# Optimization experiments

Measured on AMD Instinct MI355X. Metric: run time of the kernel, lower is better.

The kernel has to match this reference:

```python
import jax, jax.numpy as jnp
import numpy as np

NB_COMP, LAT_DIM, OUT_DIM, N = 16, 128, 512, 16384


def setup_inputs() -> dict:
    key = jax.random.key(0)
    ks = jax.random.split(key, 8)
    eps = jax.random.normal(ks[0], (N, LAT_DIM), dtype=jnp.float32)
    c = jax.random.randint(ks[1], (N,), 0, NB_COMP, dtype=jnp.int32)
    mu = jax.random.normal(ks[2], (NB_COMP, LAT_DIM), dtype=jnp.float32)
    sigma = jax.random.uniform(ks[3], (NB_COMP, LAT_DIM), dtype=jnp.float32)
    # Kaiming-ish init for the two expert linear layers
    W1 = jax.random.normal(ks[4], (NB_COMP, OUT_DIM, LAT_DIM), dtype=jnp.float32) / np.sqrt(LAT_DIM)
    b1 = jax.random.normal(ks[5], (NB_COMP, OUT_DIM), dtype=jnp.float32) * 0.01
    W2 = jax.random.normal(ks[6], (NB_COMP, OUT_DIM, OUT_DIM), dtype=jnp.float32) / np.sqrt(OUT_DIM)
    b2 = jax.random.normal(ks[7], (NB_COMP, OUT_DIM), dtype=jnp.float32) * 0.01
    return {"n": N, "eps": eps, "c": c, "mu": mu, "sigma": sigma,
            "W1": W1, "b1": b1, "W2": W2, "b2": b2}


def reference(n, eps, c, mu, sigma, W1, b1, W2, b2):
    # Per-sample latent from its component's mean-field variational dist:
    # lat[k] = eps[k] * sigma[c[k]] + mu[c[k]]
    lat = eps * sigma[c] + mu[c]                                  # (n, lat_dim)
    # Run every expert's 2-layer MLP densely, then select per-sample expert.
    hidden = jax.nn.relu(jnp.einsum("nd,chd->cnh", lat, W1) + b1[:, None, :])  # (C, n, H)
    out_all = jnp.einsum("cnh,cwh->cnw", hidden, W2) + b2[:, None, :]          # (C, n, W)
    return out_all[c, jnp.arange(n)]                              # (n, weights_dim)
```

## Files before the change

kernel.cpp:

```cpp
#include <hip/hip_runtime.h>

#define NB 16
#define LD 128
#define OD 512
#define NS 16384
#define NMB (NS/64 + NB)

typedef __attribute__((ext_vector_type(8))) short short8;
typedef __attribute__((ext_vector_type(4))) float f32x4;

#define WS_OFF     128
#define WS_POFF    256
#define WS_PERM    1024
#define WS_W1B     (128*1024)
#define WS_W2B     (WS_W1B + 2*1024*1024)
#define WS_HID     (WS_W2B + 8*1024*1024)

static __device__ __forceinline__ unsigned short f2bf(float f) {
  unsigned int u = __float_as_uint(f);
  u += 0x7FFFu + ((u >> 16) & 1u);
  return (unsigned short)(u >> 16);
}

#define SORT_T 1024
#define SORT_CH (NS / SORT_T)
__global__ __launch_bounds__(SORT_T) void k_sort(
    const int* __restrict__ c, int* __restrict__ off, int* __restrict__ poff,
    int* __restrict__ perm) {
  __shared__ int cnt[NB * SORT_T];
  __shared__ int totals[NB];
  __shared__ int ebase[NB];

  const int t = threadIdx.x;
  for (int e = 0; e < NB; ++e) cnt[e * SORT_T + t] = 0;
  __syncthreads();

  int myc[SORT_CH];
  for (int i = 0; i < SORT_CH; ++i) {
    int e = c[t * SORT_CH + i];
    myc[i] = e;
    cnt[e * SORT_T + t]++;
  }
  __syncthreads();

  const int w = t >> 6, l = t & 63;
  {
    int carry = 0;
    for (int chunk = 0; chunk < SORT_T / 64; ++chunk) {
      int idx = chunk * 64 + l;
      int v0 = cnt[w * SORT_T + idx];
      int v = v0;
      for (int d = 1; d < 64; d <<= 1) {
        int n = __shfl_up(v, d);
        if (l >= d) v += n;
      }
      cnt[w * SORT_T + idx] = carry + (v - v0);
      carry += __shfl(v, 63);
    }
    if (l == 0) totals[w] = carry;
  }
  __syncthreads();

  if (t == 0) {
    int o = 0, p = 0;
    for (int e = 0; e < NB; ++e) {
      off[e] = o; poff[e] = p; ebase[e] = o;
      o += totals[e];
      p += ((totals[e] + 63) >> 6) << 6;
    }
    off[NB] = o; poff[NB] = p;
  }
  __syncthreads();

  for (int i = 0; i < SORT_CH; ++i) {
    int e = myc[i];
    int pos = ebase[e] + cnt[e * SORT_T + t]++;
    perm[pos] = t * SORT_CH + i;
  }
}

__global__ void k_conv(const float* __restrict__ W1, const float* __restrict__ W2,
                       unsigned short* __restrict__ W1b, unsigned short* __restrict__ W2b) {
  const int n1 = NB * OD * LD / 4, n2 = NB * OD * OD / 4;
  for (int i = blockIdx.x * blockDim.x + threadIdx.x; i < n1 + n2;
       i += gridDim.x * blockDim.x) {
    float4 v; unsigned short* dst;
    if (i < n1) { v = ((const float4*)W1)[i]; dst = W1b + (size_t)i * 4; }
    else        { v = ((const float4*)W2)[i - n1]; dst = W2b + (size_t)(i - n1) * 4; }
    ushort4 o = make_ushort4(f2bf(v.x), f2bf(v.y), f2bf(v.z), f2bf(v.w));
    *(ushort4*)dst = o;
  }
}

__global__ __launch_bounds__(256) void k_gemm1(
    const float* __restrict__ eps, const float* __restrict__ mu,
    const float* __restrict__ sigma, const float* __restrict__ b1,
    const unsigned short* __restrict__ W1b,
    const int* __restrict__ off, const int* __restrict__ poff,
    const int* __restrict__ perm, unsigned short* __restrict__ hidden) {
  __shared__ alignas(16) unsigned short As[64 * 136];
  __shared__ alignas(16) unsigned short Bs[64 * 136];
  __shared__ alignas(16) float s_sig[LD];
  __shared__ alignas(16) float s_mu[LD];

  const int mt = blockIdx.y, ct = blockIdx.x;
  const int pr0 = mt * 64;
  if (pr0 >= poff[NB]) return;
  int e = 0;
  while (e < NB - 1 && poff[e + 1] <= pr0) e++;
  const int off_e = off[e];
  const int cnt   = off[e + 1] - off_e;
  const int l0    = pr0 - poff[e];

  const int t = threadIdx.x;
  if (t < LD) s_sig[t] = sigma[e * LD + t];
  else if (t < 2 * LD) s_mu[t - LD] = mu[e * LD + (t - LD)];
  __syncthreads();

  const int r = t >> 2, cseg = (t & 3) * 32;
  {
    int lrow = l0 + r;
    int k = (lrow < cnt) ? perm[off_e + lrow] : 0;
    const f32x4* eps4 = (const f32x4*)(eps + (size_t)k * LD + cseg);
    for (int j = 0; j < 8; ++j) {
      f32x4 v  = eps4[j];
      f32x4 sg = *(const f32x4*)(s_sig + cseg + j * 4);
      f32x4 m  = *(const f32x4*)(s_mu + cseg + j * 4);
      v = v * sg + m;
      ushort4 o = make_ushort4(f2bf(v[0]), f2bf(v[1]), f2bf(v[2]), f2bf(v[3]));
      *(ushort4*)(As + r * 136 + cseg + j * 4) = o;
    }
    const unsigned short* w1row =
        W1b + ((size_t)e * OD + ct * 64 + r) * LD + cseg;
    for (int j = 0; j < 4; ++j)
      *(uint4*)(Bs + r * 136 + cseg + j * 8) = *(const uint4*)(w1row + j * 8);
  }
  __syncthreads();

  const int lane = t & 63, w = t >> 6;
  const int wr = w >> 1, wc = w & 1;
  const int fr = lane & 15, fg = lane >> 4;
  f32x4 acc[2][2] = {};
  for (int ks = 0; ks < 4; ++ks) {
    short8 a[2], b[2];
    for (int fm = 0; fm < 2; ++fm)
      a[fm] = *(const short8*)(As + (wr * 32 + fm * 16 + fr) * 136 + ks * 32 + fg * 8);
    for (int fn = 0; fn < 2; ++fn)
      b[fn] = *(const short8*)(Bs + (wc * 32 + fn * 16 + fr) * 136 + ks * 32 + fg * 8);
    for (int fm = 0; fm < 2; ++fm)
      for (int fn = 0; fn < 2; ++fn)
        acc[fm][fn] = __builtin_amdgcn_mfma_f32_16x16x32_bf16(a[fm], b[fn], acc[fm][fn], 0, 0, 0);
  }

  const int colb = ct * 64 + wc * 32;
  float bv[2];
  bv[0] = b1[e * OD + colb + fr];
  bv[1] = b1[e * OD + colb + 16 + fr];
  for (int fm = 0; fm < 2; ++fm) {
    const int row0 = pr0 + wr * 32 + fm * 16 + fg * 4;
    for (int j = 0; j < 4; ++j)
      for (int fn = 0; fn < 2; ++fn) {
        float vv = acc[fm][fn][j] + bv[fn];
        vv = fmaxf(vv, 0.f);
        hidden[(size_t)(row0 + j) * OD + colb + fn * 16 + fr] = f2bf(vv);
      }
  }
}

__global__ __launch_bounds__(256) void k_gemm2(
    const float* __restrict__ b2, const unsigned short* __restrict__ W2b,
    const unsigned short* __restrict__ hidden,
    const int* __restrict__ off, const int* __restrict__ poff,
    const int* __restrict__ perm, float* __restrict__ out) {
  __shared__ alignas(16) unsigned short As[64 * 136];
  __shared__ alignas(16) unsigned short Bs[64 * 136];

  const int mt = blockIdx.y, ct = blockIdx.x;
  const int pr0 = mt * 64;
  if (pr0 >= poff[NB]) return;
  int e = 0;
  while (e < NB - 1 && poff[e + 1] <= pr0) e++;
  const int off_e = off[e];
  const int cnt   = off[e + 1] - off_e;
  const int l0    = pr0 - poff[e];

  const int t = threadIdx.x, r = t >> 2, cseg = (t & 3) * 32;
  const int lane = t & 63, w = t >> 6;
  const int wr = w >> 1, wc = w & 1;
  const int fr = lane & 15, fg = lane >> 4;

  f32x4 acc[2][2] = {};
  for (int kt = 0; kt < 4; ++kt) {
    const unsigned short* ap = hidden + (size_t)(pr0 + r) * OD + kt * 128 + cseg;
    const unsigned short* bp =
        W2b + ((size_t)e * OD + ct * 64 + r) * OD + kt * 128 + cseg;
    for (int j = 0; j < 4; ++j) {
      uint4 va = *(const uint4*)(ap + j * 8);
      uint4 vb = *(const uint4*)(bp + j * 8);
      *(uint4*)(As + r * 136 + cseg + j * 8) = va;
      *(uint4*)(Bs + r * 136 + cseg + j * 8) = vb;
    }
    __syncthreads();
    for (int ks = 0; ks < 4; ++ks) {
      short8 a[2], b[2];
      for (int fm = 0; fm < 2; ++fm)
        a[fm] = *(const short8*)(As + (wr * 32 + fm * 16 + fr) * 136 + ks * 32 + fg * 8);
      for (int fn = 0; fn < 2; ++fn)
        b[fn] = *(const short8*)(Bs + (wc * 32 + fn * 16 + fr) * 136 + ks * 32 + fg * 8);
      for (int fm = 0; fm < 2; ++fm)
        for (int fn = 0; fn < 2; ++fn)
          acc[fm][fn] = __builtin_amdgcn_mfma_f32_16x16x32_bf16(a[fm], b[fn], acc[fm][fn], 0, 0, 0);
    }
    __syncthreads();
  }

  const int colb = ct * 64 + wc * 32;
  float bv[2];
  bv[0] = b2[e * OD + colb + fr];
  bv[1] = b2[e * OD + colb + 16 + fr];
  for (int fm = 0; fm < 2; ++fm) {
    const int rl0 = wr * 32 + fm * 16 + fg * 4;
    for (int j = 0; j < 4; ++j) {
      const int lr = l0 + rl0 + j;
      if (lr < cnt) {
        const int k = perm[off_e + lr];
        for (int fn = 0; fn < 2; ++fn)
          out[(size_t)k * OD + colb + fn * 16 + fr] = acc[fm][fn][j] + bv[fn];
      }
    }
  }
}

extern "C" void kernel_launch(void* const* d_in, const int* in_sizes, int n_in,
                              void* d_out, int out_size, void* d_ws, size_t ws_size,
                              hipStream_t stream) {
  const float* eps   = (const float*)d_in[1];
  const int*   c     = (const int*)d_in[2];
  const float* mu    = (const float*)d_in[3];
  const float* sigma = (const float*)d_in[4];
  const float* W1    = (const float*)d_in[5];
  const float* b1    = (const float*)d_in[6];
  const float* W2    = (const float*)d_in[7];
  const float* b2    = (const float*)d_in[8];
  float* out = (float*)d_out;
  char*  ws  = (char*)d_ws;

  int* off     = (int*)(ws + WS_OFF);
  int* poff    = (int*)(ws + WS_POFF);
  int* perm    = (int*)(ws + WS_PERM);
  unsigned short* W1b = (unsigned short*)(ws + WS_W1B);
  unsigned short* W2b = (unsigned short*)(ws + WS_W2B);
  unsigned short* hid = (unsigned short*)(ws + WS_HID);

  k_sort<<<1, SORT_T, 0, stream>>>(c, off, poff, perm);
  k_conv<<<2048, 256, 0, stream>>>(W1, W2, W1b, W2b);
  k_gemm1<<<dim3(8, NMB), 256, 0, stream>>>(eps, mu, sigma, b1, W1b, off, poff, perm, hid);
  k_gemm2<<<dim3(8, NMB), 256, 0, stream>>>(b2, W2b, hid, off, poff, perm, out);
}
```

Before: 78.93 us.

## Use 128x128 tiles with direct global-to-LDS loads and a separate latent kernel

Grows each GEMM block tile from 64x64 to 128x128, with a 4x4 MFMA fragment grid per wave, and pads expert groups to 128 rows. Shared-memory tiles are now filled with global_load_lds instead of going through registers. The latent computation and gather move into a new k_lat kernel that writes permuted bf16 latents, so gemm1 becomes a plain tiled GEMM. The goal is more data reuse per block and less register traffic, at the cost of more padding rows, an extra launch and an unpadded, possibly bank-conflicting LDS layout.

Measured after the change: 71.69 us. -9.2%, faster.

```diff
diff --git a/kernel.cpp b/kernel.cpp
--- a/kernel.cpp
+++ b/kernel.cpp
@@ -4,7 +4,8 @@
 #define LD 128
 #define OD 512
 #define NS 16384
-#define NMB (NS/64 + NB)
+#define NPMAX (NS + NB*128)
+#define NMT (NPMAX/128)
 
 typedef __attribute__((ext_vector_type(8))) short short8;
 typedef __attribute__((ext_vector_type(4))) float f32x4;
@@ -15,6 +16,11 @@
 #define WS_W1B     (128*1024)
 #define WS_W2B     (WS_W1B + 2*1024*1024)
 #define WS_HID     (WS_W2B + 8*1024*1024)
+#define WS_LAT     (WS_HID + 20*1024*1024)
+
+#define GLDS16(g, l) __builtin_amdgcn_global_load_lds( \
+    (const __attribute__((address_space(1))) unsigned int*)(g), \
+    (__attribute__((address_space(3))) unsigned int*)(l), 16, 0, 0)
 
 static __device__ __forceinline__ unsigned short f2bf(float f) {
   unsigned int u = __float_as_uint(f);
@@ -66,7 +72,7 @@
     for (int e = 0; e < NB; ++e) {
       off[e] = o; poff[e] = p; ebase[e] = o;
       o += totals[e];
-      p += ((totals[e] + 63) >> 6) << 6;
+      p += ((totals[e] + 127) >> 7) << 7;
     }
     off[NB] = o; poff[NB] = p;
   }
@@ -92,19 +98,106 @@
   }
 }
 
+__global__ __launch_bounds__(256) void k_lat(
+    const float* __restrict__ eps, const float* __restrict__ mu,
+    const float* __restrict__ sigma,
+    const int* __restrict__ off, const int* __restrict__ poff,
+    const int* __restrict__ perm, unsigned short* __restrict__ lat) {
+  const int p0 = blockIdx.x * 8;
+  if (p0 >= poff[NB]) return;
+  int e = 0;
+  while (e < NB - 1 && poff[e + 1] <= p0) e++;
+  const int off_e = off[e], cnt = off[e + 1] - off_e;
+  const int t = threadIdx.x;
+  const int p = p0 + (t >> 5), col = (t & 31) * 4;
+  const int lrow = p - poff[e];
+  ushort4 o;
+  if (lrow < cnt) {
+    int src = perm[off_e + lrow];
+    float4 v  = *(const float4*)(eps + (size_t)src * LD + col);
+    float4 sg = *(const float4*)(sigma + e * LD + col);
+    float4 m  = *(const float4*)(mu + e * LD + col);
+    o = make_ushort4(f2bf(v.x * sg.x + m.x), f2bf(v.y * sg.y + m.y),
+                     f2bf(v.z * sg.z + m.z), f2bf(v.w * sg.w + m.w));
+  } else {
+    o = make_ushort4(0, 0, 0, 0);
+  }
+  *(ushort4*)(lat + (size_t)p * LD + col) = o;
+}
+
 __global__ __launch_bounds__(256) void k_gemm1(
-    const float* __restrict__ eps, const float* __restrict__ mu,
-    const float* __restrict__ sigma, const float* __restrict__ b1,
-    const unsigned short* __restrict__ W1b,
+    const float* __restrict__ b1, const unsigned short* __restrict__ W1b,
+    const unsigned short* __restrict__ lat,
+    const int* __restrict__ poff, unsigned short* __restrict__ hidden) {
+  __shared__ alignas(16) unsigned short As[128 * 64];
+  __shared__ alignas(16) unsigned short Bs[128 * 64];
+
+  const int mt = blockIdx.y, ct = blockIdx.x;
+  const int pr0 = mt * 128;
+  if (pr0 >= poff[NB]) return;
+  int e = 0;
+  while (e < NB - 1 && poff[e + 1] <= pr0) e++;
+
+  const int t = threadIdx.x, w = t >> 6, lane = t & 63;
+  const int wr = w >> 1, wc = w & 1;
+  const int fr = lane & 15, fg = lane >> 4;
+  const int srow = lane >> 3, scol = (lane & 7) * 8;
+
+  f32x4 acc[4][4] = {};
+  for (int kt = 0; kt < 2; ++kt) {
+#pragma unroll
+    for (int i = 0; i < 4; ++i) {
+      const int ci = w * 4 + i;
+      const int row = ci * 8 + srow;
+      GLDS16(lat + (size_t)(pr0 + row) * LD + kt * 64 + scol, As + ci * 512);
+      GLDS16(W1b + ((size_t)e * OD + ct * 128 + row) * LD + kt * 64 + scol, Bs + ci * 512);
+    }
+    __syncthreads();
+#pragma unroll
+    for (int ks = 0; ks < 2; ++ks) {
+      short8 a[4], b[4];
+#pragma unroll
+      for (int fm = 0; fm < 4; ++fm)
+        a[fm] = *(const short8*)(As + (wr * 64 + fm * 16 + fr) * 64 + ks * 32 + fg * 8);
+#pragma unroll
+      for (int fn = 0; fn < 4; ++fn)
+        b[fn] = *(const short8*)(Bs + (wc * 64 + fn * 16 + fr) * 64 + ks * 32 + fg * 8);
+#pragma unroll
+      for (int fm = 0; fm < 4; ++fm)
+#pragma unroll
+        for (int fn = 0; fn < 4; ++fn)
+          acc[fm][fn] = __builtin_amdgcn_mfma_f32_16x16x32_bf16(a[fm], b[fn], acc[fm][fn], 0, 0, 0);
+    }
+    __syncthreads();
+  }
+
+  const int colb = ct * 128 + wc * 64;
+  float bias[4];
+#pragma unroll
+  for (int fn = 0; fn < 4; ++fn) bias[fn] = b1[e * OD + colb + fn * 16 + fr];
+#pragma unroll
+  for (int fm = 0; fm < 4; ++fm) {
+    const int row0 = pr0 + wr * 64 + fm * 16 + fg * 4;
+#pragma unroll
+    for (int j = 0; j < 4; ++j) {
+      unsigned short* hrow = hidden + (size_t)(row0 + j) * OD + colb;
+#pragma unroll
+      for (int fn = 0; fn < 4; ++fn)
+        hrow[fn * 16 + fr] = f2bf(fmaxf(acc[fm][fn][j] + bias[fn], 0.f));
+    }
+  }
+}
+
+__global__ __launch_bounds__(256) void k_gemm2(
+    const float* __restrict__ b2, const unsigned short* __restrict__ W2b,
+    const unsigned short* __restrict__ hidden,
     const int* __restrict__ off, const int* __restrict__ poff,
-    const int* __restrict__ perm, unsigned short* __restrict__ hidden) {
-  __shared__ alignas(16) unsigned short As[64 * 136];
-  __shared__ alignas(16) unsigned short Bs[64 * 136];
-  __shared__ alignas(16) float s_sig[LD];
-  __shared__ alignas(16) float s_mu[LD];
+    const int* __restrict__ perm, float* __restrict__ out) {
+  __shared__ alignas(16) unsigned short As[128 * 64];
+  __shared__ alignas(16) unsigned short Bs[128 * 64];
 
   const int mt = blockIdx.y, ct = blockIdx.x;
-  const int pr0 = mt * 64;
+  const int pr0 = mt * 128;
   if (pr0 >= poff[NB]) return;
   int e = 0;
   while (e < NB - 1 && poff[e + 1] <= pr0) e++;
@@ -112,120 +205,55 @@
   const int cnt   = off[e + 1] - off_e;
   const int l0    = pr0 - poff[e];
 
-  const int t = threadIdx.x;
-  if (t < LD) s_sig[t] = sigma[e * LD + t];
-  else if (t < 2 * LD) s_mu[t - LD] = mu[e * LD + (t - LD)];
-  __syncthreads();
-
-  const int r = t >> 2, cseg = (t & 3) * 32;
-  {
-    int lrow = l0 + r;
-    int k = (lrow < cnt) ? perm[off_e + lrow] : 0;
-    const f32x4* eps4 = (const f32x4*)(eps + (size_t)k * LD + cseg);
-    for (int j = 0; j < 8; ++j) {
-      f32x4 v  = eps4[j];
-      f32x4 sg = *(const f32x4*)(s_sig + cseg + j * 4);
-      f32x4 m  = *(const f32x4*)(s_mu + cseg + j * 4);
-      v = v * sg + m;
-      ushort4 o = make_ushort4(f2bf(v[0]), f2bf(v[1]), f2bf(v[2]), f2bf(v[3]));
-      *(ushort4*)(As + r * 136 + cseg + j * 4) = o;
-    }
-    const unsigned short* w1row =
-        W1b + ((size_t)e * OD + ct * 64 + r) * LD + cseg;
-    for (int j = 0; j < 4; ++j)
-      *(uint4*)(Bs + r * 136 + cseg + j * 8) = *(const uint4*)(w1row + j * 8);
-  }
-  __syncthreads();
-
-  const int lane = t & 63, w = t >> 6;
+  const int t = threadIdx.x, w = t >> 6, lane = t & 63;
   const int wr = w >> 1, wc = w & 1;
   const int fr = lane & 15, fg = lane >> 4;
-  f32x4 acc[2][2] = {};
-  for (int ks = 0; ks < 4; ++ks) {
-    short8 a[2], b[2];
-    for (int fm = 0; fm < 2; ++fm)
-      a[fm] = *(const short8*)(As + (wr * 32 + fm * 16 + fr) * 136 + ks * 32 + fg * 8);
-    for (int fn = 0; fn < 2; ++fn)
-      b[fn] = *(const short8*)(Bs + (wc * 32 + fn * 16 + fr) * 136 + ks * 32 + fg * 8);
-    for (int fm = 0; fm < 2; ++fm)
-      for (int fn = 0; fn < 2; ++fn)
-        acc[fm][fn] = __builtin_amdgcn_mfma_f32_16x16x32_bf16(a[fm], b[fn], acc[fm][fn], 0, 0, 0);
-  }
-
-  const int colb = ct * 64 + wc * 32;
-  float bv[2];
-  bv[0] = b1[e * OD + colb + fr];
-  bv[1] = b1[e * OD + colb + 16 + fr];
-  for (int fm = 0; fm < 2; ++fm) {
-    const int row0 = pr0 + wr * 32 + fm * 16 + fg * 4;
-    for (int j = 0; j < 4; ++j)
-      for (int fn = 0; fn < 2; ++fn) {
-        float vv = acc[fm][fn][j] + bv[fn];
-        vv = fmaxf(vv, 0.f);
-        hidden[(size_t)(row0 + j) * OD + colb + fn * 16 + fr] = f2bf(vv);
-      }
-  }
-}
-
-__global__ __launch_bounds__(256) void k_gemm2(
-    const float* __restrict__ b2, const unsigned short* __restrict__ W2b,
-    const unsigned short* __restrict__ hidden,
-    const int* __restrict__ off, const int* __restrict__ poff,
-    const int* __restrict__ perm, float* __restrict__ out) {
-  __shared__ alignas(16) unsigned short As[64 * 136];
-  __shared__ alignas(16) unsigned short Bs[64 * 136];
-
-  const int mt = blockIdx.y, ct = blockIdx.x;
-  const int pr0 = mt * 64;
-  if (pr0 >= poff[NB]) return;
-  int e = 0;
-  while (e < NB - 1 && poff[e + 1] <= pr0) e++;
-  const int off_e = off[e];
-  const int cnt   = off[e + 1] - off_e;
-  const int l0    = pr0 - poff[e];
-
-  const int t = threadIdx.x, r = t >> 2, cseg = (t & 3) * 32;
-  const int lane = t & 63, w = t >> 6;
-  const int wr = w >> 1, wc = w & 1;
-  const int fr = lane & 15, fg = lane >> 4;
-
-  f32x4 acc[2][2] = {};
-  for (int kt = 0; kt < 4; ++kt) {
-    const unsigned short* ap = hidden + (size_t)(pr0 + r) * OD + kt * 128 + cseg;
-    const unsigned short* bp =
-        W2b + ((size_t)e * OD + ct * 64 + r) * OD + kt * 128 + cseg;
-    for (int j = 0; j < 4; ++j) {
-      uint4 va = *(const uint4*)(ap + j * 8);
-      uint4 vb = *(const uint4*)(bp + j * 8);
-      *(uint4*)(As + r * 136 + cseg + j * 8) = va;
-      *(uint4*)(Bs + r * 136 + cseg + j * 8) = vb;
-    }
-    __syncthreads();
-    for (int ks = 0; ks < 4; ++ks) {
-      short8 a[2], b[2];
-      for (int fm = 0; fm < 2; ++fm)
-        a[fm] = *(const short8*)(As + (wr * 32 + fm * 16 + fr) * 136 + ks * 32 + fg * 8);
-      for (int fn = 0; fn < 2; ++fn)
-        b[fn] = *(const short8*)(Bs + (wc * 32 + fn * 16 + fr) * 136 + ks * 32 + fg * 8);
-      for (int fm = 0; fm < 2; ++fm)
-        for (int fn = 0; fn < 2; ++fn)
+  const int srow = lane >> 3, scol = (lane & 7) * 8;
+
+  f32x4 acc[4][4] = {};
+  for (int kt = 0; kt < 8; ++kt) {
+#pragma unroll
+    for (int i = 0; i < 4; ++i) {
+      const int ci = w * 4 + i;
+      const int row = ci * 8 + srow;
+      GLDS16(hidden + (size_t)(pr0 + row) * OD + kt * 64 + scol, As + ci * 512);
+      GLDS16(W2b + ((size_t)e * OD + ct * 128 + row) * OD + kt * 64 + scol, Bs + ci * 512);
+    }
+    __syncthreads();
+#pragma unroll
+    for (int ks = 0; ks < 2; ++ks) {
+      short8 a[4], b[4];
+#pragma unroll
+      for (int fm = 0; fm < 4; ++fm)
+        a[fm] = *(const short8*)(As + (wr * 64 + fm * 16 + fr) * 64 + ks * 32 + fg * 8);
+#pragma unroll
+      for (int fn = 0; fn < 4; ++fn)
+        b[fn] = *(const short8*)(Bs + (wc * 64 + fn * 16 + fr) * 64 + ks * 32 + fg * 8);
+#pragma unroll
+      for (int fm = 0; fm < 4; ++fm)
+#pragma unroll
+        for (int fn = 0; fn < 4; ++fn)
           acc[fm][fn] = __builtin_amdgcn_mfma_f32_16x16x32_bf16(a[fm], b[fn], acc[fm][fn], 0, 0, 0);
     }
     __syncthreads();
   }
 
-  const int colb = ct * 64 + wc * 32;
-  float bv[2];
-  bv[0] = b2[e * OD + colb + fr];
-  bv[1] = b2[e * OD + colb + 16 + fr];
-  for (int fm = 0; fm < 2; ++fm) {
-    const int rl0 = wr * 32 + fm * 16 + fg * 4;
+  const int colb = ct * 128 + wc * 64;
+  float bias[4];
+#pragma unroll
+  for (int fn = 0; fn < 4; ++fn) bias[fn] = b2[e * OD + colb + fn * 16 + fr];
+#pragma unroll
+  for (int fm = 0; fm < 4; ++fm) {
+    const int rl0 = wr * 64 + fm * 16 + fg * 4;
+#pragma unroll
     for (int j = 0; j < 4; ++j) {
       const int lr = l0 + rl0 + j;
       if (lr < cnt) {
         const int k = perm[off_e + lr];
-        for (int fn = 0; fn < 2; ++fn)
-          out[(size_t)k * OD + colb + fn * 16 + fr] = acc[fm][fn][j] + bv[fn];
+        float* orow = out + (size_t)k * OD + colb;
+#pragma unroll
+        for (int fn = 0; fn < 4; ++fn)
+          orow[fn * 16 + fr] = acc[fm][fn][j] + bias[fn];
       }
     }
   }
@@ -251,9 +279,11 @@
   unsigned short* W1b = (unsigned short*)(ws + WS_W1B);
   unsigned short* W2b = (unsigned short*)(ws + WS_W2B);
   unsigned short* hid = (unsigned short*)(ws + WS_HID);
-
+  unsigned short* lat = (unsigned short*)(ws + WS_LAT);
+
+  k_conv<<<2048, 256, 0, stream>>>(W1, W2, W1b, W2b);
   k_sort<<<1, SORT_T, 0, stream>>>(c, off, poff, perm);
-  k_conv<<<2048, 256, 0, stream>>>(W1, W2, W1b, W2b);
-  k_gemm1<<<dim3(8, NMB), 256, 0, stream>>>(eps, mu, sigma, b1, W1b, off, poff, perm, hid);
-  k_gemm2<<<dim3(8, NMB), 256, 0, stream>>>(b2, W2b, hid, off, poff, perm, out);
-}
+  k_lat<<<NPMAX / 8, 256, 0, stream>>>(eps, mu, sigma, off, poff, perm, lat);
+  k_gemm1<<<dim3(4, NMT), 256, 0, stream>>>(b1, W1b, lat, poff, hid);
+  k_gemm2<<<dim3(4, NMT), 256, 0, stream>>>(b2, W2b, hid, off, poff, perm, out);
+}
```
